# Performance work log

Measured on AMD Instinct MI355X. Metric: run time of the kernel, lower is better.

The kernel has to match this reference:

```python
import jax, jax.numpy as jnp
import numpy as np

B, L, D_IN, D_OUT, H = 2, 2048, 1024, 1024, 16
HD = D_OUT // H


def setup_inputs() -> dict:
    key = jax.random.key(0)
    ks = jax.random.split(key, 7)
    s_in = 1.0 / np.sqrt(D_IN)
    s_out = 1.0 / np.sqrt(D_OUT)
    return {
        "x": jax.random.normal(ks[0], (B, L, D_IN), dtype=jnp.float32),
        "Wq": jax.random.uniform(ks[1], (D_OUT, D_IN), jnp.float32, -s_in, s_in),
        "Wg": jax.random.uniform(ks[2], (D_OUT, D_IN), jnp.float32, -s_in, s_in),
        "Wk": jax.random.uniform(ks[3], (D_OUT, D_IN), jnp.float32, -s_in, s_in),
        "Wv": jax.random.uniform(ks[4], (D_OUT, D_IN), jnp.float32, -s_in, s_in),
        "Wo": jax.random.uniform(ks[5], (D_OUT, D_OUT), jnp.float32, -s_out, s_out),
        "bo": jax.random.uniform(ks[6], (D_OUT,), jnp.float32, -s_out, s_out),
    }


def reference(x, Wq, Wg, Wk, Wv, Wo, bo):
    b, l, _ = x.shape
    # projections (torch Linear: x @ W^T)
    q = jnp.einsum('bld,od->blo', x, Wq).reshape(b, l, H, HD)
    g = jnp.einsum('bld,od->blo', x, Wg)
    k = jnp.einsum('bld,od->blo', x, Wk).reshape(b, l, H, HD)
    v = jnp.einsum('bld,od->blo', x, Wv).reshape(b, l, H, HD)
    # attention scores [B,H,L,L]
    scores = jnp.einsum('bqhd,bkhd->bhqk', q, k)
    causal = jnp.tril(jnp.ones((l, l), dtype=bool))
    neg = jnp.finfo(scores.dtype).min
    scores = jnp.where(causal[None, None], scores, neg)
    attn = jax.nn.softmax(scores / np.sqrt(HD), axis=-1)
    ctx = jnp.einsum('bhqk,bkhd->bqhd', attn, v).reshape(b, l, D_OUT)
    ctx = ctx * jax.nn.sigmoid(g)
    return jnp.einsum('blo,po->blp', ctx, Wo) + bo
```

## Files before the change

### kernel.cpp

```cpp
#include <hip/hip_runtime.h>
#include <hip/hip_bf16.h>


typedef __bf16 v8bf __attribute__((ext_vector_type(8)));
typedef __bf16 v4bf __attribute__((ext_vector_type(4)));
typedef float  v4f  __attribute__((ext_vector_type(4)));

using gas_void = const __attribute__((address_space(1))) void*;
using las_void = __attribute__((address_space(3))) void*;

__device__ __forceinline__ void async_ld16(const void* g, void* l) {
  __builtin_amdgcn_global_load_lds((gas_void)g, (las_void)l, 16, 0, 0);
}
__device__ __forceinline__ float fexp2(float x) { return __builtin_amdgcn_exp2f(x); }

#define QSCALE 0.18033688011112042f
#define LOG2E  1.4426950408889634f
#define FIXMAX 8.0f

__global__ void cvt_all_kernel(const float* __restrict__ x,  const float* __restrict__ Wq,
                               const float* __restrict__ Wg, const float* __restrict__ Wk,
                               const float* __restrict__ Wv, const float* __restrict__ Wo,
                               __bf16* __restrict__ xb, __bf16* __restrict__ w3,
                               __bf16* __restrict__ wvb, __bf16* __restrict__ wob) {
  int i = blockIdx.x * 256 + threadIdx.x;
  const float* s; v4bf* d; int j; float sc = 1.f;
  if (i < 1048576)      { s = x;  d = (v4bf*)xb;           j = i; }
  else if (i < 1310720) { s = Wq; d = (v4bf*)w3;           j = i - 1048576; sc = QSCALE; }
  else if (i < 1572864) { s = Wg; d = (v4bf*)w3 + 262144;  j = i - 1310720; }
  else if (i < 1835008) { s = Wk; d = (v4bf*)w3 + 524288;  j = i - 1572864; }
  else if (i < 2097152) { s = Wv; d = (v4bf*)wvb;          j = i - 1835008; }
  else                  { s = Wo; d = (v4bf*)wob;          j = i - 2097152; }
  float4 v = reinterpret_cast<const float4*>(s)[j];
  v4bf o;
  o[0] = (__bf16)(v.x * sc); o[1] = (__bf16)(v.y * sc);
  o[2] = (__bf16)(v.z * sc); o[3] = (__bf16)(v.w * sc);
  d[j] = o;
}

template<bool OUTF32, int BN>
__global__ __launch_bounds__(256) void gemm_bt_kernel(
    const __bf16* __restrict__ A, const __bf16* __restrict__ B,
    void* __restrict__ C, const float* __restrict__ bias,
    int K, int lda, int ldb, int ldc) {
  constexpr int NI = BN / 32;
  __shared__ __bf16 As[128 * 32];
  __shared__ __bf16 Bs[BN * 32];
  const int tid  = threadIdx.x;
  const int w    = tid >> 6;
  const int lane = tid & 63;
  const int fr   = lane & 15;
  const int fq   = lane >> 4;
  const int srow = lane >> 2;
  const int scol = lane & 3;
  const int m0 = blockIdx.y * 128, n0 = blockIdx.x * BN;
  const int wr = (w >> 1) * 64, wc = (w & 1) * (BN / 2);

  v4f acc[4][NI];
#pragma unroll
  for (int i = 0; i < 4; ++i)
#pragma unroll
    for (int j = 0; j < NI; ++j)
#pragma unroll
      for (int r = 0; r < 4; ++r) acc[i][j][r] = 0.f;

  for (int k0 = 0; k0 < K; k0 += 32) {
#pragma unroll
    for (int i = 0; i < 2; ++i) {
      const int c = w + i * 4;
      async_ld16(A + (size_t)(m0 + c * 16 + srow) * lda + k0 + scol * 8, (void*)(As + c * 512));
    }
#pragma unroll
    for (int i = 0; i < BN / 64; ++i) {
      const int c = w + i * 4;
      async_ld16(B + (size_t)(n0 + c * 16 + srow) * ldb + k0 + scol * 8, (void*)(Bs + c * 512));
    }
    __syncthreads();

    v8bf a[4], b[NI];
#pragma unroll
    for (int mi = 0; mi < 4; ++mi)
      a[mi] = *reinterpret_cast<const v8bf*>(As + (wr + mi * 16 + fr) * 32 + fq * 8);
#pragma unroll
    for (int ni = 0; ni < NI; ++ni)
      b[ni] = *reinterpret_cast<const v8bf*>(Bs + (wc + ni * 16 + fr) * 32 + fq * 8);
#pragma unroll
    for (int mi = 0; mi < 4; ++mi)
#pragma unroll
      for (int ni = 0; ni < NI; ++ni)
        acc[mi][ni] = __builtin_amdgcn_mfma_f32_16x16x32_bf16(a[mi], b[ni], acc[mi][ni], 0, 0, 0);
    __syncthreads();
  }

#pragma unroll
  for (int mi = 0; mi < 4; ++mi)
#pragma unroll
    for (int ni = 0; ni < NI; ++ni)
#pragma unroll
      for (int r = 0; r < 4; ++r) {
        const int row = m0 + wr + mi * 16 + fq * 4 + r;
        const int col = n0 + wc + ni * 16 + fr;
        const float v = acc[mi][ni][r];
        if (OUTF32) {
          reinterpret_cast<float*>(C)[(size_t)row * ldc + col] = v + bias[col];
        } else {
          reinterpret_cast<__bf16*>(C)[(size_t)row * ldc + col] = (__bf16)v;
        }
      }
}

__global__ __launch_bounds__(256, 2) void attn_kernel(
    const __bf16* __restrict__ QGK, const __bf16* __restrict__ VT,
    __bf16* __restrict__ CTX) {
  constexpr int LD = 3072, L = 2048;
  __shared__ __align__(16) char lds[53760];
  const int w = threadIdx.x >> 6, lane = threadIdx.x & 63;
  const int fr = lane & 15, fq = lane >> 4;
  const int tl = w >> 1, hf = w & 1;
  const int orig = ((blockIdx.x & 7) << 6) | (blockIdx.x >> 3);
  const int bh = orig >> 4, jj = orig & 15;
  const int b = bh >> 4, h = bh & 15, hb = h * 64;
  const __bf16* base  = QGK + (size_t)b * L * LD;
  const __bf16* vbase = VT + (size_t)hb * 4096 + (size_t)b * L;
  __bf16* pw = (__bf16*)(lds + 32768 + w * 2560);
  float* comb = (float*)(lds + 32768);

  v8bf onev;
#pragma unroll
  for (int i = 0; i < 8; ++i) onev[i] = (__bf16)1.0f;

  for (int ph = 0; ph < 2; ++ph) {
    const int g  = ph ? 31 - jj : jj;
    const int qt = 2 * g + tl, q0 = qt * 32, nkt = g + 1;

    v4f cacc[2][4], csum[2];
#pragma unroll
    for (int mi = 0; mi < 2; ++mi) {
#pragma unroll
      for (int r = 0; r < 4; ++r) csum[mi][r] = 0.f;
#pragma unroll
      for (int nf = 0; nf < 4; ++nf)
#pragma unroll
        for (int r = 0; r < 4; ++r) cacc[mi][nf][r] = 0.f;
    }

    v8bf qf[2][2];
#pragma unroll
    for (int mi = 0; mi < 2; ++mi)
#pragma unroll
      for (int ks = 0; ks < 2; ++ks)
        qf[mi][ks] = *reinterpret_cast<const v8bf*>(
            base + (size_t)(q0 + mi * 16 + fr) * LD + hb + ks * 32 + fq * 8);

    auto stage = [&](int bi, int k0s) {
      char* bf_ = bi ? (char*)lds + 16384 : (char*)lds;
#pragma unroll
      for (int i = 0; i < 2; ++i) {
        const int slot = i * 256 + w * 64 + lane;
        const int r = slot >> 3;
        const int cc = ((slot & 7) ^ (r & 7)) * 8;
        async_ld16(base + (size_t)(k0s + r) * LD + 2048 + hb + cc,
                   bf_ + (i * 256 + w * 64) * 16);
        async_ld16(vbase + (size_t)r * 4096 + k0s + cc,
                   bf_ + 8192 + (i * 256 + w * 64) * 16);
      }
    };

    stage(0, 0);
    for (int kt = 0; kt < nkt; ++kt) {
      if (kt + 1 < nkt) {
        stage((kt + 1) & 1, (kt + 1) * 64);
        asm volatile("s_waitcnt vmcnt(4)" ::: "memory");
      } else {
        asm volatile("s_waitcnt vmcnt(0)" ::: "memory");
      }
      __builtin_amdgcn_s_barrier();
      __builtin_amdgcn_sched_barrier(0);
      const bool last = (kt == nkt - 1);
      if (!(last && tl == 0 && hf == 1)) {
        const int k0 = kt * 64;
        const __bf16* Kt = (const __bf16*)(kt & 1 ? lds + 16384 : lds);
        const __bf16* Vt = Kt + 4096;
        v8bf kf[2][2], vf[4];
#pragma unroll
        for (int ks = 0; ks < 2; ++ks)
#pragma unroll
          for (int nj = 0; nj < 2; ++nj)
            kf[ks][nj] = *reinterpret_cast<const v8bf*>(
                Kt + ((2 * hf + nj) * 16 + fr) * 64 + (((ks * 4 + fq) ^ (fr & 7)) * 8));
#pragma unroll
        for (int nf = 0; nf < 4; ++nf)
          vf[nf] = *reinterpret_cast<const v8bf*>(
              Vt + (nf * 16 + fr) * 64 + (((hf * 4 + fq) ^ (fr & 7)) * 8));

        v4f s[2][2];
#pragma unroll
        for (int mi = 0; mi < 2; ++mi)
#pragma unroll
          for (int nj = 0; nj < 2; ++nj)
#pragma unroll
            for (int r = 0; r < 4; ++r) s[mi][nj][r] = 0.f;
#pragma unroll
        for (int ks = 0; ks < 2; ++ks)
#pragma unroll
          for (int mi = 0; mi < 2; ++mi)
#pragma unroll
            for (int nj = 0; nj < 2; ++nj)
              s[mi][nj] = __builtin_amdgcn_mfma_f32_16x16x32_bf16(
                  kf[ks][nj], qf[mi][ks], s[mi][nj], 0, 0, 0);

        const bool mask = last && (hf == tl);
#pragma unroll
        for (int mi = 0; mi < 2; ++mi) {
          const int qrow = q0 + mi * 16 + fr;
#pragma unroll
          for (int nj = 0; nj < 2; ++nj) {
            const int kvb = k0 + hf * 32 + nj * 16 + fq * 4;
            v4bf pk;
#pragma unroll
            for (int r = 0; r < 4; ++r) {
              float sv = s[mi][nj][r];
              if (mask && (kvb + r > qrow)) sv = -__builtin_inff();
              pk[r] = (__bf16)fexp2(sv - FIXMAX);
            }
            *reinterpret_cast<v4bf*>(pw + (mi * 16 + fr) * 40 + nj * 16 + fq * 4) = pk;
          }
        }

        v8bf pa[2];
#pragma unroll
        for (int mi = 0; mi < 2; ++mi)
          pa[mi] = *reinterpret_cast<const v8bf*>(pw + (mi * 16 + fr) * 40 + fq * 8);
#pragma unroll
        for (int mi = 0; mi < 2; ++mi)
          csum[mi] = __builtin_amdgcn_mfma_f32_16x16x32_bf16(pa[mi], onev, csum[mi], 0, 0, 0);
#pragma unroll
        for (int nf = 0; nf < 4; ++nf)
#pragma unroll
          for (int mi = 0; mi < 2; ++mi)
            cacc[mi][nf] = __builtin_amdgcn_mfma_f32_16x16x32_bf16(pa[mi], vf[nf], cacc[mi][nf], 0, 0, 0);
      }
      __builtin_amdgcn_sched_barrier(0);
      __builtin_amdgcn_s_barrier();
    }

    __syncthreads();
    const bool writer = (hf != ph);
    float* slot = comb + (tl * 64 + lane) * 41;
    if (writer) {
#pragma unroll
      for (int mi = 0; mi < 2; ++mi) {
#pragma unroll
        for (int nf = 0; nf < 4; ++nf)
#pragma unroll
          for (int r = 0; r < 4; ++r) slot[mi * 16 + nf * 4 + r] = cacc[mi][nf][r];
#pragma unroll
        for (int r = 0; r < 4; ++r) slot[32 + mi * 4 + r] = csum[mi][r];
      }
    }
    __syncthreads();
    if (!writer) {
#pragma unroll
      for (int mi = 0; mi < 2; ++mi) {
#pragma unroll
        for (int nf = 0; nf < 4; ++nf)
#pragma unroll
          for (int r = 0; r < 4; ++r) cacc[mi][nf][r] += slot[mi * 16 + nf * 4 + r];
#pragma unroll
        for (int r = 0; r < 4; ++r) csum[mi][r] += slot[32 + mi * 4 + r];
      }
#pragma unroll
      for (int mi = 0; mi < 2; ++mi)
#pragma unroll
        for (int r = 0; r < 4; ++r) {
          const int grow = q0 + mi * 16 + fq * 4 + r;
          const float rl = 1.f / csum[mi][r];
#pragma unroll
          for (int nf = 0; nf < 4; ++nf) {
            const int col = hb + nf * 16 + fr;
            float v = cacc[mi][nf][r] * rl;
            const float gt = (float)base[(size_t)grow * LD + 1024 + col];
            v *= 1.f / (1.f + fexp2(-gt * LOG2E));
            CTX[((size_t)b * L + grow) * 1024 + col] = (__bf16)v;
          }
        }
    }
  }
}

extern "C" void kernel_launch(void* const* d_in, const int* in_sizes, int n_in,
                              void* d_out, int out_size, void* d_ws, size_t ws_size,
                              hipStream_t stream) {
  const float* x  = (const float*)d_in[0];
  const float* Wq = (const float*)d_in[1];
  const float* Wg = (const float*)d_in[2];
  const float* Wk = (const float*)d_in[3];
  const float* Wv = (const float*)d_in[4];
  const float* Wo = (const float*)d_in[5];
  const float* bo = (const float*)d_in[6];

  char* ws = (char*)d_ws;
  __bf16* xb  = (__bf16*)(ws);
  __bf16* w3  = (__bf16*)(ws + (8u  << 20));
  __bf16* wvb = (__bf16*)(ws + (14u << 20));
  __bf16* wob = (__bf16*)(ws + (16u << 20));
  __bf16* qgk = (__bf16*)(ws + (18u << 20));
  __bf16* vt  = (__bf16*)(ws + (42u << 20));
  __bf16* ctx = (__bf16*)(ws + (50u << 20));

  cvt_all_kernel<<<dim3(9216), dim3(256), 0, stream>>>(x, Wq, Wg, Wk, Wv, Wo,
                                                       xb, w3, wvb, wob);

  gemm_bt_kernel<false, 128><<<dim3(24, 32), dim3(256), 0, stream>>>(
      xb, w3, (void*)qgk, nullptr, 1024, 1024, 1024, 3072);

  gemm_bt_kernel<false, 64><<<dim3(64, 8), dim3(256), 0, stream>>>(
      wvb, xb, (void*)vt, nullptr, 1024, 1024, 1024, 4096);

  attn_kernel<<<dim3(512), dim3(256), 0, stream>>>(qgk, vt, ctx);

  gemm_bt_kernel<true, 64><<<dim3(16, 32), dim3(256), 0, stream>>>(
      ctx, wob, d_out, bo, 1024, 1024, 1024, 1024);
}
```

Before: 127.2 us.

## Merge QGK and V projections into one launch; split attention into per-tile 2-wave blocks

Combines the QGK and V^T projection GEMMs into a single launch of 1024 blocks using a shared device tile function, with the V GEMM now using 128-wide tiles. The attention kernel changes from 512 blocks of 4 waves, each processing two paired query tiles, to 2048 blocks of 2 waves, one per 32-row query tile, launched heaviest-first. K is still staged through double-buffered LDS, but V fragments are now read straight from global memory, and MFMA sections run at raised wave priority. The aim is fewer launches, better occupancy and load balance, at the cost of uncoalesced global V reads and less K reuse per block.

Measured after the change: 159.7 us. 25.5% more time.

```diff
diff --git a/kernel.cpp b/kernel.cpp
--- a/kernel.cpp
+++ b/kernel.cpp
@@ -39,13 +39,12 @@
 }
 
 template<bool OUTF32, int BN>
-__global__ __launch_bounds__(256) void gemm_bt_kernel(
+__device__ __forceinline__ void gemm_tile(
     const __bf16* __restrict__ A, const __bf16* __restrict__ B,
     void* __restrict__ C, const float* __restrict__ bias,
-    int K, int lda, int ldb, int ldc) {
+    int K, int lda, int ldb, int ldc, int m0, int n0,
+    __bf16* As, __bf16* Bs) {
   constexpr int NI = BN / 32;
-  __shared__ __bf16 As[128 * 32];
-  __shared__ __bf16 Bs[BN * 32];
   const int tid  = threadIdx.x;
   const int w    = tid >> 6;
   const int lane = tid & 63;
@@ -53,7 +52,6 @@
   const int fq   = lane >> 4;
   const int srow = lane >> 2;
   const int scol = lane & 3;
-  const int m0 = blockIdx.y * 128, n0 = blockIdx.x * BN;
   const int wr = (w >> 1) * 64, wc = (w & 1) * (BN / 2);
 
   v4f acc[4][NI];
@@ -109,182 +107,209 @@
       }
 }
 
-__global__ __launch_bounds__(256, 2) void attn_kernel(
+__global__ __launch_bounds__(256) void proj_kernel(
+    const __bf16* __restrict__ xb, const __bf16* __restrict__ w3,
+    const __bf16* __restrict__ wvb, __bf16* __restrict__ qgk, __bf16* __restrict__ vt) {
+  __shared__ __bf16 As[128 * 32];
+  __shared__ __bf16 Bs[128 * 32];
+  const int bid = blockIdx.x;
+  if (bid < 768) {
+    gemm_tile<false, 128>(xb, w3, (void*)qgk, nullptr, 1024, 1024, 1024, 3072,
+                          (bid / 24) * 128, (bid % 24) * 128, As, Bs);
+  } else {
+    const int t = bid - 768;
+    gemm_tile<false, 128>(wvb, xb, (void*)vt, nullptr, 1024, 1024, 1024, 4096,
+                          (t >> 5) * 128, (t & 31) * 128, As, Bs);
+  }
+}
+
+template<bool OUTF32, int BN>
+__global__ __launch_bounds__(256) void gemm_bt_kernel(
+    const __bf16* __restrict__ A, const __bf16* __restrict__ B,
+    void* __restrict__ C, const float* __restrict__ bias,
+    int K, int lda, int ldb, int ldc) {
+  __shared__ __bf16 As[128 * 32];
+  __shared__ __bf16 Bs[BN * 32];
+  gemm_tile<OUTF32, BN>(A, B, C, bias, K, lda, ldb, ldc,
+                        blockIdx.y * 128, blockIdx.x * BN, As, Bs);
+}
+
+__global__ __launch_bounds__(128, 4) void attn_kernel(
     const __bf16* __restrict__ QGK, const __bf16* __restrict__ VT,
     __bf16* __restrict__ CTX) {
   constexpr int LD = 3072, L = 2048;
-  __shared__ __align__(16) char lds[53760];
+  __shared__ __align__(16) char lds[21504];
   const int w = threadIdx.x >> 6, lane = threadIdx.x & 63;
   const int fr = lane & 15, fq = lane >> 4;
-  const int tl = w >> 1, hf = w & 1;
-  const int orig = ((blockIdx.x & 7) << 6) | (blockIdx.x >> 3);
-  const int bh = orig >> 4, jj = orig & 15;
+  const int bid = blockIdx.x;
+  const int qt = 63 - (bid >> 5);
+  const int bh = bid & 31;
   const int b = bh >> 4, h = bh & 15, hb = h * 64;
+  const int q0 = qt * 32;
+  const int nkt = (qt >> 1) + 1;
   const __bf16* base  = QGK + (size_t)b * L * LD;
   const __bf16* vbase = VT + (size_t)hb * 4096 + (size_t)b * L;
-  __bf16* pw = (__bf16*)(lds + 32768 + w * 2560);
-  float* comb = (float*)(lds + 32768);
+  __bf16* pw = (__bf16*)(lds + 16384 + w * 2560);
 
   v8bf onev;
 #pragma unroll
   for (int i = 0; i < 8; ++i) onev[i] = (__bf16)1.0f;
 
-  for (int ph = 0; ph < 2; ++ph) {
-    const int g  = ph ? 31 - jj : jj;
-    const int qt = 2 * g + tl, q0 = qt * 32, nkt = g + 1;
-
-    v4f cacc[2][4], csum[2];
+  v8bf qf[2][2];
+#pragma unroll
+  for (int mi = 0; mi < 2; ++mi)
+#pragma unroll
+    for (int ks = 0; ks < 2; ++ks)
+      qf[mi][ks] = *reinterpret_cast<const v8bf*>(
+          base + (size_t)(q0 + mi * 16 + fr) * LD + hb + ks * 32 + fq * 8);
+
+  v4f cacc[2][4], csum[2];
+#pragma unroll
+  for (int mi = 0; mi < 2; ++mi) {
+#pragma unroll
+    for (int r = 0; r < 4; ++r) csum[mi][r] = 0.f;
+#pragma unroll
+    for (int nf = 0; nf < 4; ++nf)
+#pragma unroll
+      for (int r = 0; r < 4; ++r) cacc[mi][nf][r] = 0.f;
+  }
+
+  auto stage = [&](int bi, int k0s) {
+    char* bf_ = (char*)lds + bi * 8192;
+#pragma unroll
+    for (int i = 0; i < 4; ++i) {
+      const int slot = i * 128 + w * 64 + lane;
+      const int r = slot >> 3;
+      const int cc = ((slot & 7) ^ (r & 7)) * 8;
+      async_ld16(base + (size_t)(k0s + r) * LD + 2048 + hb + cc,
+                 bf_ + (i * 128 + w * 64) * 16);
+    }
+  };
+
+  stage(0, 0);
+  for (int kt = 0; kt < nkt; ++kt) {
+    const int k0 = kt * 64;
+    const bool last = (kt == nkt - 1);
+    v8bf vf[4];
+#pragma unroll
+    for (int nf = 0; nf < 4; ++nf)
+      vf[nf] = *reinterpret_cast<const v8bf*>(
+          vbase + (size_t)(nf * 16 + fr) * 4096 + k0 + w * 32 + fq * 8);
+    if (!last) {
+      stage((kt + 1) & 1, k0 + 64);
+      asm volatile("s_waitcnt vmcnt(8)" ::: "memory");
+    } else {
+      asm volatile("s_waitcnt vmcnt(4)" ::: "memory");
+    }
+    __builtin_amdgcn_s_barrier();
+    __builtin_amdgcn_sched_barrier(0);
+
+    if (!(last && !(qt & 1) && w == 1)) {
+      const __bf16* Kt = (const __bf16*)(lds + (kt & 1) * 8192);
+      v8bf kf[2][2];
+#pragma unroll
+      for (int ks = 0; ks < 2; ++ks)
+#pragma unroll
+        for (int nj = 0; nj < 2; ++nj)
+          kf[ks][nj] = *reinterpret_cast<const v8bf*>(
+              Kt + (w * 32 + nj * 16 + fr) * 64 + (((ks * 4 + fq) ^ (fr & 7)) * 8));
+
+      v4f s[2][2];
+#pragma unroll
+      for (int mi = 0; mi < 2; ++mi)
+#pragma unroll
+        for (int nj = 0; nj < 2; ++nj)
+#pragma unroll
+          for (int r = 0; r < 4; ++r) s[mi][nj][r] = 0.f;
+      __builtin_amdgcn_s_setprio(1);
+#pragma unroll
+      for (int ks = 0; ks < 2; ++ks)
+#pragma unroll
+        for (int mi = 0; mi < 2; ++mi)
+#pragma unroll
+          for (int nj = 0; nj < 2; ++nj)
+            s[mi][nj] = __builtin_amdgcn_mfma_f32_16x16x32_bf16(
+                kf[ks][nj], qf[mi][ks], s[mi][nj], 0, 0, 0);
+      __builtin_amdgcn_s_setprio(0);
+
+      const bool mask = last && (w == (qt & 1));
+#pragma unroll
+      for (int mi = 0; mi < 2; ++mi) {
+        const int qrow = q0 + mi * 16 + fr;
+#pragma unroll
+        for (int nj = 0; nj < 2; ++nj) {
+          const int kvb = k0 + w * 32 + nj * 16 + fq * 4;
+          v4bf pk;
+#pragma unroll
+          for (int r = 0; r < 4; ++r) {
+            float sv = s[mi][nj][r];
+            if (mask && (kvb + r > qrow)) sv = -__builtin_inff();
+            pk[r] = (__bf16)fexp2(sv - FIXMAX);
+          }
+          *reinterpret_cast<v4bf*>(pw + (mi * 16 + fr) * 40 + nj * 16 + fq * 4) = pk;
+        }
+      }
+
+      v8bf pa[2];
+#pragma unroll
+      for (int mi = 0; mi < 2; ++mi)
+        pa[mi] = *reinterpret_cast<const v8bf*>(pw + (mi * 16 + fr) * 40 + fq * 8);
+      __builtin_amdgcn_s_setprio(1);
+#pragma unroll
+      for (int mi = 0; mi < 2; ++mi)
+        csum[mi] = __builtin_amdgcn_mfma_f32_16x16x32_bf16(pa[mi], onev, csum[mi], 0, 0, 0);
+#pragma unroll
+      for (int nf = 0; nf < 4; ++nf)
+#pragma unroll
+        for (int mi = 0; mi < 2; ++mi)
+          cacc[mi][nf] = __builtin_amdgcn_mfma_f32_16x16x32_bf16(pa[mi], vf[nf], cacc[mi][nf], 0, 0, 0);
+      __builtin_amdgcn_s_setprio(0);
+    }
+    __builtin_amdgcn_sched_barrier(0);
+    __builtin_amdgcn_s_barrier();
+  }
+
+  __syncthreads();
+  float* comb = (float*)lds;
+  if (w == 1) {
+    float* slot = comb + lane * 41;
 #pragma unroll
     for (int mi = 0; mi < 2; ++mi) {
 #pragma unroll
-      for (int r = 0; r < 4; ++r) csum[mi][r] = 0.f;
-#pragma unroll
       for (int nf = 0; nf < 4; ++nf)
 #pragma unroll
-        for (int r = 0; r < 4; ++r) cacc[mi][nf][r] = 0.f;
-    }
-
-    v8bf qf[2][2];
+        for (int r = 0; r < 4; ++r) slot[mi * 16 + nf * 4 + r] = cacc[mi][nf][r];
+#pragma unroll
+      for (int r = 0; r < 4; ++r) slot[32 + mi * 4 + r] = csum[mi][r];
+    }
+  }
+  __syncthreads();
+  if (w == 0) {
+    const float* slot = comb + lane * 41;
+#pragma unroll
+    for (int mi = 0; mi < 2; ++mi) {
+#pragma unroll
+      for (int nf = 0; nf < 4; ++nf)
+#pragma unroll
+        for (int r = 0; r < 4; ++r) cacc[mi][nf][r] += slot[mi * 16 + nf * 4 + r];
+#pragma unroll
+      for (int r = 0; r < 4; ++r) csum[mi][r] += slot[32 + mi * 4 + r];
+    }
 #pragma unroll
     for (int mi = 0; mi < 2; ++mi)
 #pragma unroll
-      for (int ks = 0; ks < 2; ++ks)
-        qf[mi][ks] = *reinterpret_cast<const v8bf*>(
-            base + (size_t)(q0 + mi * 16 + fr) * LD + hb + ks * 32 + fq * 8);
-
-    auto stage = [&](int bi, int k0s) {
-      char* bf_ = bi ? (char*)lds + 16384 : (char*)lds;
-#pragma unroll
-      for (int i = 0; i < 2; ++i) {
-        const int slot = i * 256 + w * 64 + lane;
-        const int r = slot >> 3;
-        const int cc = ((slot & 7) ^ (r & 7)) * 8;
-        async_ld16(base + (size_t)(k0s + r) * LD + 2048 + hb + cc,
-                   bf_ + (i * 256 + w * 64) * 16);
-        async_ld16(vbase + (size_t)r * 4096 + k0s + cc,
-                   bf_ + 8192 + (i * 256 + w * 64) * 16);
+      for (int r = 0; r < 4; ++r) {
+        const int grow = q0 + mi * 16 + fq * 4 + r;
+        const float rl = 1.f / csum[mi][r];
+#pragma unroll
+        for (int nf = 0; nf < 4; ++nf) {
+          const int col = hb + nf * 16 + fr;
+          float v = cacc[mi][nf][r] * rl;
+          const float gt = (float)base[(size_t)grow * LD + 1024 + col];
+          v *= 1.f / (1.f + fexp2(-gt * LOG2E));
+          CTX[((size_t)b * L + grow) * 1024 + col] = (__bf16)v;
+        }
       }
-    };
-
-    stage(0, 0);
-    for (int kt = 0; kt < nkt; ++kt) {
-      if (kt + 1 < nkt) {
-        stage((kt + 1) & 1, (kt + 1) * 64);
-        asm volatile("s_waitcnt vmcnt(4)" ::: "memory");
-      } else {
-        asm volatile("s_waitcnt vmcnt(0)" ::: "memory");
-      }
-      __builtin_amdgcn_s_barrier();
-      __builtin_amdgcn_sched_barrier(0);
-      const bool last = (kt == nkt - 1);
-      if (!(last && tl == 0 && hf == 1)) {
-        const int k0 = kt * 64;
-        const __bf16* Kt = (const __bf16*)(kt & 1 ? lds + 16384 : lds);
-        const __bf16* Vt = Kt + 4096;
-        v8bf kf[2][2], vf[4];
-#pragma unroll
-        for (int ks = 0; ks < 2; ++ks)
-#pragma unroll
-          for (int nj = 0; nj < 2; ++nj)
-            kf[ks][nj] = *reinterpret_cast<const v8bf*>(
-                Kt + ((2 * hf + nj) * 16 + fr) * 64 + (((ks * 4 + fq) ^ (fr & 7)) * 8));
-#pragma unroll
-        for (int nf = 0; nf < 4; ++nf)
-          vf[nf] = *reinterpret_cast<const v8bf*>(
-              Vt + (nf * 16 + fr) * 64 + (((hf * 4 + fq) ^ (fr & 7)) * 8));
-
-        v4f s[2][2];
-#pragma unroll
-        for (int mi = 0; mi < 2; ++mi)
-#pragma unroll
-          for (int nj = 0; nj < 2; ++nj)
-#pragma unroll
-            for (int r = 0; r < 4; ++r) s[mi][nj][r] = 0.f;
-#pragma unroll
-        for (int ks = 0; ks < 2; ++ks)
-#pragma unroll
-          for (int mi = 0; mi < 2; ++mi)
-#pragma unroll
-            for (int nj = 0; nj < 2; ++nj)
-              s[mi][nj] = __builtin_amdgcn_mfma_f32_16x16x32_bf16(
-                  kf[ks][nj], qf[mi][ks], s[mi][nj], 0, 0, 0);
-
-        const bool mask = last && (hf == tl);
-#pragma unroll
-        for (int mi = 0; mi < 2; ++mi) {
-          const int qrow = q0 + mi * 16 + fr;
-#pragma unroll
-          for (int nj = 0; nj < 2; ++nj) {
-            const int kvb = k0 + hf * 32 + nj * 16 + fq * 4;
-            v4bf pk;
-#pragma unroll
-            for (int r = 0; r < 4; ++r) {
-              float sv = s[mi][nj][r];
-              if (mask && (kvb + r > qrow)) sv = -__builtin_inff();
-              pk[r] = (__bf16)fexp2(sv - FIXMAX);
-            }
-            *reinterpret_cast<v4bf*>(pw + (mi * 16 + fr) * 40 + nj * 16 + fq * 4) = pk;
-          }
-        }
-
-        v8bf pa[2];
-#pragma unroll
-        for (int mi = 0; mi < 2; ++mi)
-          pa[mi] = *reinterpret_cast<const v8bf*>(pw + (mi * 16 + fr) * 40 + fq * 8);
-#pragma unroll
-        for (int mi = 0; mi < 2; ++mi)
-          csum[mi] = __builtin_amdgcn_mfma_f32_16x16x32_bf16(pa[mi], onev, csum[mi], 0, 0, 0);
-#pragma unroll
-        for (int nf = 0; nf < 4; ++nf)
-#pragma unroll
-          for (int mi = 0; mi < 2; ++mi)
-            cacc[mi][nf] = __builtin_amdgcn_mfma_f32_16x16x32_bf16(pa[mi], vf[nf], cacc[mi][nf], 0, 0, 0);
-      }
-      __builtin_amdgcn_sched_barrier(0);
-      __builtin_amdgcn_s_barrier();
-    }
-
-    __syncthreads();
-    const bool writer = (hf != ph);
-    float* slot = comb + (tl * 64 + lane) * 41;
-    if (writer) {
-#pragma unroll
-      for (int mi = 0; mi < 2; ++mi) {
-#pragma unroll
-        for (int nf = 0; nf < 4; ++nf)
-#pragma unroll
-          for (int r = 0; r < 4; ++r) slot[mi * 16 + nf * 4 + r] = cacc[mi][nf][r];
-#pragma unroll
-        for (int r = 0; r < 4; ++r) slot[32 + mi * 4 + r] = csum[mi][r];
-      }
-    }
-    __syncthreads();
-    if (!writer) {
-#pragma unroll
-      for (int mi = 0; mi < 2; ++mi) {
-#pragma unroll
-        for (int nf = 0; nf < 4; ++nf)
-#pragma unroll
-          for (int r = 0; r < 4; ++r) cacc[mi][nf][r] += slot[mi * 16 + nf * 4 + r];
-#pragma unroll
-        for (int r = 0; r < 4; ++r) csum[mi][r] += slot[32 + mi * 4 + r];
-      }
-#pragma unroll
-      for (int mi = 0; mi < 2; ++mi)
-#pragma unroll
-        for (int r = 0; r < 4; ++r) {
-          const int grow = q0 + mi * 16 + fq * 4 + r;
-          const float rl = 1.f / csum[mi][r];
-#pragma unroll
-          for (int nf = 0; nf < 4; ++nf) {
-            const int col = hb + nf * 16 + fr;
-            float v = cacc[mi][nf][r] * rl;
-            const float gt = (float)base[(size_t)grow * LD + 1024 + col];
-            v *= 1.f / (1.f + fexp2(-gt * LOG2E));
-            CTX[((size_t)b * L + grow) * 1024 + col] = (__bf16)v;
-          }
-        }
-    }
   }
 }
 
@@ -311,13 +336,9 @@
   cvt_all_kernel<<<dim3(9216), dim3(256), 0, stream>>>(x, Wq, Wg, Wk, Wv, Wo,
                                                        xb, w3, wvb, wob);
 
-  gemm_bt_kernel<false, 128><<<dim3(24, 32), dim3(256), 0, stream>>>(
-      xb, w3, (void*)qgk, nullptr, 1024, 1024, 1024, 3072);
-
-  gemm_bt_kernel<false, 64><<<dim3(64, 8), dim3(256), 0, stream>>>(
-      wvb, xb, (void*)vt, nullptr, 1024, 1024, 1024, 4096);
-
-  attn_kernel<<<dim3(512), dim3(256), 0, stream>>>(qgk, vt, ctx);
+  proj_kernel<<<dim3(1024), dim3(256), 0, stream>>>(xb, w3, wvb, qgk, vt);
+
+  attn_kernel<<<dim3(2048), dim3(128), 0, stream>>>(qgk, vt, ctx);
 
   gemm_bt_kernel<true, 64><<<dim3(16, 32), dim3(256), 0, stream>>>(
       ctx, wob, d_out, bo, 1024, 1024, 1024, 1024);
```
